# Kernel tuning notes

Measured on AMD Instinct MI355X. Metric: run time of the kernel, lower is better.

Reference implementation:

```python
import jax, jax.numpy as jnp
import numpy as np

DIM, HEADS, WS, SHIFT = 192, 6, 8, 4
EPS = 1e-5


def layer_norm(x, g, b):
    mu = jnp.mean(x, axis=-1, keepdims=True)
    var = jnp.mean(jnp.square(x - mu), axis=-1, keepdims=True)
    return (x - mu) * jax.lax.rsqrt(var + EPS) * g + b


def window_partition(x, ws):
    # x: [B, H, W, C] -> [B*nW, ws*ws, C]
    B, H, W, C = x.shape
    x = x.reshape(B, H // ws, ws, W // ws, ws, C)
    return x.transpose(0, 1, 3, 2, 4, 5).reshape(-1, ws * ws, C)


def window_merge(win, ws, B, H, W, C):
    x = win.reshape(B, H // ws, W // ws, ws, ws, C)
    return x.transpose(0, 1, 3, 2, 4, 5).reshape(B, H, W, C)


def make_shift_mask(H, W, ws, shift):
    # standard Swin attention mask for shifted windows (host-side constant)
    img = np.zeros((H, W), dtype=np.float32)
    cnt = 0
    slices = (slice(0, -ws), slice(-ws, -shift), slice(-shift, None))
    for hs in slices:
        for wsl in slices:
            img[hs, wsl] = cnt
            cnt += 1
    m = img.reshape(H // ws, ws, W // ws, ws).transpose(0, 2, 1, 3).reshape(-1, ws * ws)  # [nW, N]
    diff = m[:, None, :] - m[:, :, None]
    return jnp.asarray(np.where(diff != 0, -100.0, 0.0).astype(np.float32))  # [nW, N, N]


def swin_attention(x, qkv_w, qkv_b, proj_w, proj_b, shift):
    B, H, W, C = x.shape
    h, d = HEADS, C // HEADS
    scale = 1.0 / jnp.sqrt(jnp.asarray(d, x.dtype))
    if shift > 0:
        x = jnp.roll(x, shift=(-shift, -shift), axis=(1, 2))
    win = window_partition(x, WS)                       # [Bn, N, C]
    Bn, N, _ = win.shape
    qkv = win @ qkv_w + qkv_b                           # [Bn, N, 3C]
    qkv = qkv.reshape(Bn, N, 3, h, d).transpose(2, 0, 3, 1, 4)
    q, k, v = qkv[0], qkv[1], qkv[2]                    # [Bn, h, N, d]
    attn = jnp.einsum('bhnd,bhmd->bhnm', q, k) * scale  # [Bn, h, N, N]
    if shift > 0:
        mask = make_shift_mask(H, W, WS, shift)         # [nW, N, N]
        nW = mask.shape[0]
        attn = attn.reshape(Bn // nW, nW, h, N, N) + mask[None, :, None]
        attn = attn.reshape(Bn, h, N, N)
    attn = jax.nn.softmax(attn, axis=-1)
    out = jnp.einsum('bhnm,bhmd->bhnd', attn, v)        # [Bn, h, N, d]
    out = out.transpose(0, 2, 1, 3).reshape(Bn, N, C)
    out = out @ proj_w + proj_b
    out = window_merge(out, WS, B, H, W, C)
    if shift > 0:
        out = jnp.roll(out, shift=(shift, shift), axis=(1, 2))
    return out


def setup_inputs() -> dict:
    key = jax.random.key(0)
    ks = jax.random.split(key, 6)
    B, H, W, C = 8, 128, 128, DIM
    s = 0.02
    return {
        'x': jax.random.normal(ks[0], (B, H, W, C), jnp.float32),
        'ln1_g': jnp.ones((C,), jnp.float32),
        'ln1_b': jnp.zeros((C,), jnp.float32),
        'qkv1_w': jax.random.normal(ks[1], (C, 3 * C), jnp.float32) * s,
        'qkv1_b': jnp.zeros((3 * C,), jnp.float32),
        'proj1_w': jax.random.normal(ks[2], (C, C), jnp.float32) * s,
        'proj1_b': jnp.zeros((C,), jnp.float32),
        'ln2_g': jnp.ones((C,), jnp.float32),
        'ln2_b': jnp.zeros((C,), jnp.float32),
        'qkv2_w': jax.random.normal(ks[3], (C, 3 * C), jnp.float32) * s,
        'qkv2_b': jnp.zeros((3 * C,), jnp.float32),
        'proj2_w': jax.random.normal(ks[4], (C, C), jnp.float32) * s,
        'proj2_b': jnp.zeros((C,), jnp.float32),
    }


def reference(x, ln1_g, ln1_b, qkv1_w, qkv1_b, proj1_w, proj1_b,
              ln2_g, ln2_b, qkv2_w, qkv2_b, proj2_w, proj2_b):
    # W-MSA branch (mlp1 is an empty Sequential -> identity)
    y = layer_norm(x, ln1_g, ln1_b)
    x = x + swin_attention(y, qkv1_w, qkv1_b, proj1_w, proj1_b, shift=0)
    # SW-MSA branch (mlp2 is identity)
    y = layer_norm(x, ln2_g, ln2_b)
    x = x + swin_attention(y, qkv2_w, qkv2_b, proj2_w, proj2_b, shift=SHIFT)
    return x
```

## Files before the change

### kernel.cpp

```cpp
#include <hip/hip_runtime.h>

typedef unsigned int   u32;
typedef unsigned short u16;
typedef __bf16 bf16x8 __attribute__((ext_vector_type(8)));
typedef float  f32x4  __attribute__((ext_vector_type(4)));

__device__ __forceinline__ u16 f2bf(float f) {
    u32 u = __builtin_bit_cast(u32, f);
    u += 0x7FFFu + ((u >> 16) & 1u);
    return (u16)(u >> 16);
}
__device__ __forceinline__ u32 cvtpk(float a, float b) {
    u32 r;
    asm("v_cvt_pk_bf16_f32 %0, %1, %2" : "=v"(r) : "v"(a), "v"(b));
    return r;
}
__device__ __forceinline__ bf16x8 ldfrag(const u16* p) {
    return __builtin_bit_cast(bf16x8, *reinterpret_cast<const uint4*>(p));
}

__device__ __forceinline__ u32 swz(u32 i) { return i ^ ((i >> 3) & 7u); }

template<int SHIFT>
__global__ __launch_bounds__(768) void swin_branch(
    const float* __restrict__ xin, float* __restrict__ xout,
    const float* __restrict__ ln_g, const float* __restrict__ ln_b,
    const u16*   __restrict__ wqkv_t,
    const float* __restrict__ qkv_b,
    const u16*   __restrict__ wproj_t,
    const float* __restrict__ proj_b)
{
    __shared__ __align__(16) u16 smem[49152];
    __shared__ float red1[2][6][64];
    __shared__ float red2[2][6][64];
    constexpr u32 QOFF = 12288;
    constexpr float QSC = 0.17677669529663689f * 1.4426950408889634f;

    const int tid  = threadIdx.x;
    const int win  = (tid >= 384) ? 1 : 0;
    const int lt   = tid - win*384;
    const int wid  = lt >> 6;
    const int lane = lt & 63;
    const int lr   = lane & 15;
    const int lg   = lane >> 4;
    const u32 lsw  = swz((u32)lane);
    const u32 SB   = (u32)win * 24576u;

    const int Wid = blockIdx.x*2 + win;
    const int b   = Wid >> 8;
    const int wy  = (Wid >> 4) & 15;
    const int wx  = Wid & 15;

    {
        const int ty = lane >> 3, tx = lane & 7;
        const int shy = (wy*8 + ty + SHIFT) & 127;
        const int shx = (wx*8 + tx + SHIFT) & 127;
        const float* xp = xin + ((size_t)((b*128 + shy)*128 + shx))*192 + wid*32;
        float xv[32];
        float s1 = 0.f, s2 = 0.f;
        #pragma unroll
        for (int j = 0; j < 8; ++j) {
            float4 v = reinterpret_cast<const float4*>(xp)[j];
            xv[j*4+0]=v.x; xv[j*4+1]=v.y; xv[j*4+2]=v.z; xv[j*4+3]=v.w;
            s1 += v.x+v.y+v.z+v.w;
            s2 += v.x*v.x + v.y*v.y + v.z*v.z + v.w*v.w;
        }
        red1[win][wid][lane] = s1; red2[win][wid][lane] = s2;
        __syncthreads();
        float a1 = 0.f, a2 = 0.f;
        #pragma unroll
        for (int w = 0; w < 6; ++w) { a1 += red1[win][w][lane]; a2 += red2[win][w][lane]; }
        const float mu = a1 * (1.f/192.f);
        const float rs = rsqrtf(a2 * (1.f/192.f) - mu*mu + 1e-5f);
        const float* gp = ln_g + wid*32;
        const float* bp = ln_b + wid*32;
        const u32 yblk = SB + (u32)((lg*6 + wid)*512);
        #pragma unroll
        for (int cc8 = 0; cc8 < 4; ++cc8) {
            u32 pk[4];
            #pragma unroll
            for (int q = 0; q < 4; ++q) {
                int j = cc8*8 + q*2;
                float y0 = (xv[j]   - mu)*rs*gp[j]   + bp[j];
                float y1 = (xv[j+1] - mu)*rs*gp[j+1] + bp[j+1];
                pk[q] = cvtpk(y0, y1);
            }
            *reinterpret_cast<uint4*>(&smem[yblk + swz((u32)(lr + 16*cc8))*8]) =
                make_uint4(pk[0],pk[1],pk[2],pk[3]);
        }
    }
    __syncthreads();

    uint2 kpk[4][2];
    uint2 vpk[4][2];
    {
        {
            f32x4 acc[4][4];
            #pragma unroll
            for (int mi=0; mi<4; ++mi)
                #pragma unroll
                for (int t=0; t<4; ++t) acc[mi][t] = f32x4{0.f,0.f,0.f,0.f};
            #pragma unroll
            for (int ks=0; ks<6; ++ks) {
                bf16x8 af[4];
                #pragma unroll
                for (int mi=0; mi<4; ++mi)
                    af[mi] = ldfrag(&smem[SB + (u32)((mi*6+ks)*512) + lsw*8]);
                bf16x8 bw[4];
                #pragma unroll
                for (int t=0; t<4; ++t)
                    bw[t] = ldfrag(&wqkv_t[((t>>1)*192 + wid*32 + (t&1)*16 + lr)*192 + 32*ks + 8*lg]);
                #pragma unroll
                for (int mi=0; mi<4; ++mi)
                    #pragma unroll
                    for (int t=0; t<4; ++t)
                        acc[mi][t] = __builtin_amdgcn_mfma_f32_16x16x32_bf16(bw[t], af[mi], acc[mi][t], 0,0,0);
            }
            #pragma unroll
            for (int t=0; t<2; ++t) {
                const float4 b4 = *reinterpret_cast<const float4*>(&qkv_b[wid*32 + t*16 + 4*lg]);
                const u32 chunk = (u32)lr + 16u*(u32)(2*t + (lg>>1));
                #pragma unroll
                for (int mi=0; mi<4; ++mi) {
                    float v0 = (acc[mi][t][0] + b4.x) * QSC;
                    float v1 = (acc[mi][t][1] + b4.y) * QSC;
                    float v2 = (acc[mi][t][2] + b4.z) * QSC;
                    float v3 = (acc[mi][t][3] + b4.w) * QSC;
                    *reinterpret_cast<uint2*>(
                        &smem[SB + QOFF + (u32)(wid*2048) + mi*512 + swz(chunk)*8 + 4*(lg&1)]) =
                        make_uint2(cvtpk(v0,v1), cvtpk(v2,v3));
                }
            }
            #pragma unroll
            for (int t2=0; t2<2; ++t2) {
                const float4 b4 = *reinterpret_cast<const float4*>(&qkv_b[192 + wid*32 + t2*16 + 4*lg]);
                #pragma unroll
                for (int mi=0; mi<4; ++mi)
                    kpk[mi][t2] = make_uint2(
                        cvtpk(acc[mi][2+t2][0] + b4.x, acc[mi][2+t2][1] + b4.y),
                        cvtpk(acc[mi][2+t2][2] + b4.z, acc[mi][2+t2][3] + b4.w));
            }
        }
        {
            f32x4 acc[4][2];
            #pragma unroll
            for (int mi=0; mi<4; ++mi)
                #pragma unroll
                for (int t=0; t<2; ++t) acc[mi][t] = f32x4{0.f,0.f,0.f,0.f};
            #pragma unroll
            for (int ks=0; ks<6; ++ks) {
                bf16x8 af[4];
                #pragma unroll
                for (int mi=0; mi<4; ++mi)
                    af[mi] = ldfrag(&smem[SB + (u32)((mi*6+ks)*512) + lsw*8]);
                bf16x8 bw[2];
                #pragma unroll
                for (int t=0; t<2; ++t)
                    bw[t] = ldfrag(&wqkv_t[(384 + wid*32 + t*16 + lr)*192 + 32*ks + 8*lg]);
                #pragma unroll
                for (int mi=0; mi<4; ++mi)
                    #pragma unroll
                    for (int t=0; t<2; ++t)
                        acc[mi][t] = __builtin_amdgcn_mfma_f32_16x16x32_bf16(af[mi], bw[t], acc[mi][t], 0,0,0);
            }
            #pragma unroll
            for (int tv=0; tv<2; ++tv) {
                const float bias = qkv_b[384 + wid*32 + tv*16 + lr];
                #pragma unroll
                for (int mi=0; mi<4; ++mi)
                    vpk[mi][tv] = make_uint2(
                        cvtpk(acc[mi][tv][0] + bias, acc[mi][tv][1] + bias),
                        cvtpk(acc[mi][tv][2] + bias, acc[mi][tv][3] + bias));
            }
        }
    }
    __syncthreads();

    float rsum[4];
    f32x4 o_[2][4];
    {
        const u32 W  = SB + (u32)(wid*512);
        const u32 QB = SB + QOFF + (u32)(wid*2048);
        #define BLK(s) ((u32)(s)*3072u + W)

        #pragma unroll
        for (int t2=0; t2<2; ++t2) {
            const u32 chunk = (u32)lr + 16u*(u32)(2*t2 + (lg>>1));
            #pragma unroll
            for (int mi=0; mi<4; ++mi)
                *reinterpret_cast<uint2*>(
                    &smem[BLK(mi) + swz(chunk)*8 + 4*(lg&1)]) = kpk[mi][t2];
        }
        bf16x8 ak[4], bq[4];
        #pragma unroll
        for (int mi=0; mi<4; ++mi) ak[mi] = ldfrag(&smem[BLK(mi) + lsw*8]);
        #pragma unroll
        for (int nq=0; nq<4; ++nq) bq[nq] = ldfrag(&smem[QB + nq*512 + lsw*8]);
        __builtin_amdgcn_sched_barrier(0);

        int qcl[4];
        if constexpr (SHIFT > 0) {
            #pragma unroll
            for (int nq=0; nq<4; ++nq) {
                const int qt = 16*nq + lr;
                const int hu = wy*8 + (qt>>3);
                const int wu = wx*8 + (qt&7);
                qcl[nq] = ((hu >= 124) ? 2 : (hu >= 120 ? 1 : 0))*3
                        + ((wu >= 124) ? 2 : (wu >= 120 ? 1 : 0));
            }
        }

        uint2 p16[4][4];
        #pragma unroll
        for (int mi=0; mi<4; ++mi) {
            f32x4 sr[4];
            #pragma unroll
            for (int nq=0; nq<4; ++nq)
                sr[nq] = __builtin_amdgcn_mfma_f32_16x16x32_bf16(ak[mi], bq[nq],
                             f32x4{0.f,0.f,0.f,0.f}, 0,0,0);
            #pragma unroll
            for (int rg=0; rg<4; ++rg) {
                int kcl = 0;
                if constexpr (SHIFT > 0) {
                    const int kt = 16*mi + 4*lg + rg;
                    const int hu = wy*8 + (kt>>3);
                    const int wu = wx*8 + (kt&7);
                    kcl = ((hu >= 124) ? 2 : (hu >= 120 ? 1 : 0))*3
                        + ((wu >= 124) ? 2 : (wu >= 120 ? 1 : 0));
                }
                #pragma unroll
                for (int nq=0; nq<4; ++nq) {
                    float e = exp2f(sr[nq][rg]);
                    if constexpr (SHIFT > 0)
                        e = (kcl == qcl[nq]) ? e : 0.f;
                    sr[nq][rg] = e;
                }
            }
            #pragma unroll
            for (int nq=0; nq<4; ++nq)
                p16[mi][nq] = make_uint2(cvtpk(sr[nq][0], sr[nq][1]),
                                         cvtpk(sr[nq][2], sr[nq][3]));
        }

        #pragma unroll
        for (int mi=0; mi<4; ++mi) {
            const u32 chunk = (u32)lr + 16u*(u32)(2*(mi&1) + (lg>>1));
            #pragma unroll
            for (int nq=0; nq<4; ++nq) {
                const u32 base = (mi >> 1) ? BLK(nq) : (QB + nq*512);
                *reinterpret_cast<uint2*>(&smem[base + swz(chunk)*8 + 4*(lg&1)]) = p16[mi][nq];
            }
        }
        bf16x8 bp[4][2];
        #pragma unroll
        for (int nq=0; nq<4; ++nq) {
            bp[nq][0] = ldfrag(&smem[QB + nq*512 + lsw*8]);
            bp[nq][1] = ldfrag(&smem[BLK(nq) + lsw*8]);
        }
        __builtin_amdgcn_sched_barrier(0);

        bf16x8 aones;
        {
            const u32 one2 = 0x3F803F80u;
            aones = __builtin_bit_cast(bf16x8, make_uint4(one2, one2, one2, one2));
        }
        #pragma unroll
        for (int nq=0; nq<4; ++nq) {
            f32x4 racc = __builtin_amdgcn_mfma_f32_16x16x32_bf16(aones, bp[nq][0],
                             f32x4{0.f,0.f,0.f,0.f}, 0,0,0);
            racc = __builtin_amdgcn_mfma_f32_16x16x32_bf16(aones, bp[nq][1], racc, 0,0,0);
            rsum[nq] = __builtin_amdgcn_rcpf(racc[0]);
        }

        #pragma unroll
        for (int mi=0; mi<4; ++mi) {
            const u32 chunk = (u32)lr + 16u*(u32)(2*(mi&1) + (lg>>1));
            #pragma unroll
            for (int tv=0; tv<2; ++tv)
                *reinterpret_cast<uint2*>(
                    &smem[QB + (u32)((2*tv + (mi>>1))*512) + swz(chunk)*8 + 4*(lg&1)]) = vpk[mi][tv];
        }
        bf16x8 av[2][2];
        #pragma unroll
        for (int dv=0; dv<2; ++dv)
            #pragma unroll
            for (int ks=0; ks<2; ++ks)
                av[dv][ks] = ldfrag(&smem[QB + (u32)((2*dv + ks)*512) + lsw*8]);
        __builtin_amdgcn_sched_barrier(0);

        #pragma unroll
        for (int dv=0; dv<2; ++dv)
            #pragma unroll
            for (int nq=0; nq<4; ++nq) {
                o_[dv][nq] = __builtin_amdgcn_mfma_f32_16x16x32_bf16(av[dv][0], bp[nq][0],
                                 f32x4{0.f,0.f,0.f,0.f}, 0,0,0);
                o_[dv][nq] = __builtin_amdgcn_mfma_f32_16x16x32_bf16(av[dv][1], bp[nq][1],
                                 o_[dv][nq], 0,0,0);
            }
        __builtin_amdgcn_sched_barrier(0);

        #pragma unroll
        for (int dv=0; dv<2; ++dv) {
            const u32 chunk = (u32)lr + 16u*(u32)(2*dv + (lg>>1));
            #pragma unroll
            for (int nq=0; nq<4; ++nq) {
                const float r = rsum[nq];
                *reinterpret_cast<uint2*>(&smem[BLK(nq) + swz(chunk)*8 + 4*(lg&1)]) =
                    make_uint2(cvtpk(o_[dv][nq][0]*r, o_[dv][nq][1]*r),
                               cvtpk(o_[dv][nq][2]*r, o_[dv][nq][3]*r));
            }
        }
        #undef BLK
    }
    __syncthreads();

    {
        f32x4 a2[4][2];
        #pragma unroll
        for (int mi=0; mi<4; ++mi)
            #pragma unroll
            for (int ni=0; ni<2; ++ni) a2[mi][ni] = f32x4{0.f,0.f,0.f,0.f};
        #pragma unroll
        for (int ks=0; ks<6; ++ks) {
            bf16x8 af[4], bw[2];
            #pragma unroll
            for (int mi=0; mi<4; ++mi)
                af[mi] = ldfrag(&smem[SB + (u32)((mi*6+ks)*512) + lsw*8]);
            #pragma unroll
            for (int ni=0; ni<2; ++ni)
                bw[ni] = ldfrag(&wproj_t[(wid*32 + 16*ni + lr)*192 + 32*ks + 8*lg]);
            #pragma unroll
            for (int mi=0; mi<4; ++mi)
                #pragma unroll
                for (int ni=0; ni<2; ++ni)
                    a2[mi][ni] = __builtin_amdgcn_mfma_f32_16x16x32_bf16(af[mi], bw[ni], a2[mi][ni], 0,0,0);
        }
        #pragma unroll
        for (int ni=0; ni<2; ++ni) {
            const int c  = wid*32 + 16*ni + lr;
            const float pb = proj_b[c];
            #pragma unroll
            for (int mi=0; mi<4; ++mi)
                #pragma unroll
                for (int rg=0; rg<4; ++rg) {
                    const int row = 16*mi + 4*lg + rg;
                    const int ty = row >> 3, tx = row & 7;
                    const int shy = (wy*8 + ty + SHIFT) & 127;
                    const int shx = (wx*8 + tx + SHIFT) & 127;
                    const size_t idx = ((size_t)((b*128 + shy)*128 + shx))*192 + c;
                    xout[idx] = xin[idx] + a2[mi][ni][rg] + pb;
                }
        }
    }
}

__global__ void prep_weights(const float* __restrict__ qkv1, const float* __restrict__ proj1,
                             const float* __restrict__ qkv2, const float* __restrict__ proj2,
                             u16* __restrict__ ws)
{
    const int i = blockIdx.x*blockDim.x + threadIdx.x;
    if (i < 110592) {
        const int n = i / 192, k = i - n*192;
        ws[i]          = f2bf(qkv1[k*576 + n]);
        ws[147456 + i] = f2bf(qkv2[k*576 + n]);
    }
    if (i < 36864) {
        const int n = i / 192, k = i - n*192;
        ws[110592 + i] = f2bf(proj1[k*192 + n]);
        ws[258048 + i] = f2bf(proj2[k*192 + n]);
    }
}

extern "C" void kernel_launch(void* const* d_in, const int* in_sizes, int n_in,
                              void* d_out, int out_size, void* d_ws, size_t ws_size,
                              hipStream_t stream)
{
    const float* x       = (const float*)d_in[0];
    const float* ln1_g   = (const float*)d_in[1];
    const float* ln1_b   = (const float*)d_in[2];
    const float* qkv1_w  = (const float*)d_in[3];
    const float* qkv1_b  = (const float*)d_in[4];
    const float* proj1_w = (const float*)d_in[5];
    const float* proj1_b = (const float*)d_in[6];
    const float* ln2_g   = (const float*)d_in[7];
    const float* ln2_b   = (const float*)d_in[8];
    const float* qkv2_w  = (const float*)d_in[9];
    const float* qkv2_b  = (const float*)d_in[10];
    const float* proj2_w = (const float*)d_in[11];
    const float* proj2_b = (const float*)d_in[12];
    float* out = (float*)d_out;
    u16*   wsp = (u16*)d_ws;

    prep_weights<<<dim3(432), dim3(256), 0, stream>>>(qkv1_w, proj1_w, qkv2_w, proj2_w, wsp);
    swin_branch<0><<<dim3(1024), dim3(768), 0, stream>>>(x,   out, ln1_g, ln1_b,
                                                         wsp,        qkv1_b, wsp+110592, proj1_b);
    swin_branch<4><<<dim3(1024), dim3(768), 0, stream>>>(out, out, ln2_g, ln2_b,
                                                         wsp+147456, qkv2_b, wsp+258048, proj2_b);
}
```

Baseline: 262.8 us.

## Make Swin branch kernel persistent and prefetch next window's input

Shrinks the grid from 1024 to 256 blocks. Each block now loops over 4 window pairs in turn. During the output-projection phase of one iteration, it issues the global loads of x for the next window pair into registers, so LayerNorm input latency overlaps with MFMA work. This removes block launch and prologue repetition, but keeps more live registers across the loop and serialises work per CU.

```diff
diff --git a/kernel.cpp b/kernel.cpp
--- a/kernel.cpp
+++ b/kernel.cpp
@@ -46,310 +46,331 @@
     const u32 lsw  = swz((u32)lane);
     const u32 SB   = (u32)win * 24576u;
 
-    const int Wid = blockIdx.x*2 + win;
-    const int b   = Wid >> 8;
-    const int wy  = (Wid >> 4) & 15;
-    const int wx  = Wid & 15;
-
+    const int ty = lane >> 3, tx = lane & 7;
+
+    float4 xv4[8];
     {
-        const int ty = lane >> 3, tx = lane & 7;
-        const int shy = (wy*8 + ty + SHIFT) & 127;
-        const int shx = (wx*8 + tx + SHIFT) & 127;
-        const float* xp = xin + ((size_t)((b*128 + shy)*128 + shx))*192 + wid*32;
-        float xv[32];
-        float s1 = 0.f, s2 = 0.f;
+        const int Wid = (int)blockIdx.x*2 + win;
+        const int b0=Wid>>8, wy0=(Wid>>4)&15, wx0=Wid&15;
+        const int shy=(wy0*8+ty+SHIFT)&127, shx=(wx0*8+tx+SHIFT)&127;
+        const float* xp = xin + ((size_t)((b0*128+shy)*128+shx))*192 + wid*32;
         #pragma unroll
-        for (int j = 0; j < 8; ++j) {
-            float4 v = reinterpret_cast<const float4*>(xp)[j];
-            xv[j*4+0]=v.x; xv[j*4+1]=v.y; xv[j*4+2]=v.z; xv[j*4+3]=v.w;
-            s1 += v.x+v.y+v.z+v.w;
-            s2 += v.x*v.x + v.y*v.y + v.z*v.z + v.w*v.w;
-        }
-        red1[win][wid][lane] = s1; red2[win][wid][lane] = s2;
+        for (int j=0;j<8;++j) xv4[j] = reinterpret_cast<const float4*>(xp)[j];
+    }
+
+    #pragma unroll 1
+    for (int it = 0; it < 4; ++it) {
+        const int Wid = (it*256 + (int)blockIdx.x)*2 + win;
+        const int b   = Wid >> 8;
+        const int wy  = (Wid >> 4) & 15;
+        const int wx  = Wid & 15;
+
+        {
+            float s1 = 0.f, s2 = 0.f;
+            #pragma unroll
+            for (int j = 0; j < 8; ++j) {
+                float4 v = xv4[j];
+                s1 += v.x+v.y+v.z+v.w;
+                s2 += v.x*v.x + v.y*v.y + v.z*v.z + v.w*v.w;
+            }
+            red1[win][wid][lane] = s1; red2[win][wid][lane] = s2;
+        }
         __syncthreads();
-        float a1 = 0.f, a2 = 0.f;
-        #pragma unroll
-        for (int w = 0; w < 6; ++w) { a1 += red1[win][w][lane]; a2 += red2[win][w][lane]; }
-        const float mu = a1 * (1.f/192.f);
-        const float rs = rsqrtf(a2 * (1.f/192.f) - mu*mu + 1e-5f);
-        const float* gp = ln_g + wid*32;
-        const float* bp = ln_b + wid*32;
-        const u32 yblk = SB + (u32)((lg*6 + wid)*512);
-        #pragma unroll
-        for (int cc8 = 0; cc8 < 4; ++cc8) {
-            u32 pk[4];
-            #pragma unroll
-            for (int q = 0; q < 4; ++q) {
-                int j = cc8*8 + q*2;
-                float y0 = (xv[j]   - mu)*rs*gp[j]   + bp[j];
-                float y1 = (xv[j+1] - mu)*rs*gp[j+1] + bp[j+1];
-                pk[q] = cvtpk(y0, y1);
-            }
-            *reinterpret_cast<uint4*>(&smem[yblk + swz((u32)(lr + 16*cc8))*8]) =
-                make_uint4(pk[0],pk[1],pk[2],pk[3]);
-        }
-    }
-    __syncthreads();
-
-    uint2 kpk[4][2];
-    uint2 vpk[4][2];
-    {
         {
-            f32x4 acc[4][4];
+            float a1 = 0.f, a2 = 0.f;
+            #pragma unroll
+            for (int w = 0; w < 6; ++w) { a1 += red1[win][w][lane]; a2 += red2[win][w][lane]; }
+            const float mu = a1 * (1.f/192.f);
+            const float rs = rsqrtf(a2 * (1.f/192.f) - mu*mu + 1e-5f);
+            const float* gp = ln_g + wid*32;
+            const float* bp = ln_b + wid*32;
+            const float* xf = reinterpret_cast<const float*>(xv4);
+            const u32 yblk = SB + (u32)((lg*6 + wid)*512);
+            #pragma unroll
+            for (int cc8 = 0; cc8 < 4; ++cc8) {
+                u32 pk[4];
+                #pragma unroll
+                for (int q = 0; q < 4; ++q) {
+                    int j = cc8*8 + q*2;
+                    float y0 = (xf[j]   - mu)*rs*gp[j]   + bp[j];
+                    float y1 = (xf[j+1] - mu)*rs*gp[j+1] + bp[j+1];
+                    pk[q] = cvtpk(y0, y1);
+                }
+                *reinterpret_cast<uint4*>(&smem[yblk + swz((u32)(lr + 16*cc8))*8]) =
+                    make_uint4(pk[0],pk[1],pk[2],pk[3]);
+            }
+        }
+        __syncthreads();
+
+        uint2 kpk[4][2];
+        uint2 vpk[4][2];
+        {
+            {
+                f32x4 acc[4][4];
+                #pragma unroll
+                for (int mi=0; mi<4; ++mi)
+                    #pragma unroll
+                    for (int t=0; t<4; ++t) acc[mi][t] = f32x4{0.f,0.f,0.f,0.f};
+                #pragma unroll
+                for (int ks=0; ks<6; ++ks) {
+                    bf16x8 af[4];
+                    #pragma unroll
+                    for (int mi=0; mi<4; ++mi)
+                        af[mi] = ldfrag(&smem[SB + (u32)((mi*6+ks)*512) + lsw*8]);
+                    bf16x8 bw[4];
+                    #pragma unroll
+                    for (int t=0; t<4; ++t)
+                        bw[t] = ldfrag(&wqkv_t[((t>>1)*192 + wid*32 + (t&1)*16 + lr)*192 + 32*ks + 8*lg]);
+                    #pragma unroll
+                    for (int mi=0; mi<4; ++mi)
+                        #pragma unroll
+                        for (int t=0; t<4; ++t)
+                            acc[mi][t] = __builtin_amdgcn_mfma_f32_16x16x32_bf16(bw[t], af[mi], acc[mi][t], 0,0,0);
+                }
+                #pragma unroll
+                for (int t=0; t<2; ++t) {
+                    const float4 b4 = *reinterpret_cast<const float4*>(&qkv_b[wid*32 + t*16 + 4*lg]);
+                    const u32 chunk = (u32)lr + 16u*(u32)(2*t + (lg>>1));
+                    #pragma unroll
+                    for (int mi=0; mi<4; ++mi) {
+                        float v0 = (acc[mi][t][0] + b4.x) * QSC;
+                        float v1 = (acc[mi][t][1] + b4.y) * QSC;
+                        float v2 = (acc[mi][t][2] + b4.z) * QSC;
+                        float v3 = (acc[mi][t][3] + b4.w) * QSC;
+                        *reinterpret_cast<uint2*>(
+                            &smem[SB + QOFF + (u32)(wid*2048) + mi*512 + swz(chunk)*8 + 4*(lg&1)]) =
+                            make_uint2(cvtpk(v0,v1), cvtpk(v2,v3));
+                    }
+                }
+                #pragma unroll
+                for (int t2=0; t2<2; ++t2) {
+                    const float4 b4 = *reinterpret_cast<const float4*>(&qkv_b[192 + wid*32 + t2*16 + 4*lg]);
+                    #pragma unroll
+                    for (int mi=0; mi<4; ++mi)
+                        kpk[mi][t2] = make_uint2(
+                            cvtpk(acc[mi][2+t2][0] + b4.x, acc[mi][2+t2][1] + b4.y),
+                            cvtpk(acc[mi][2+t2][2] + b4.z, acc[mi][2+t2][3] + b4.w));
+                }
+            }
+            {
+                f32x4 acc[4][2];
+                #pragma unroll
+                for (int mi=0; mi<4; ++mi)
+                    #pragma unroll
+                    for (int t=0; t<2; ++t) acc[mi][t] = f32x4{0.f,0.f,0.f,0.f};
+                #pragma unroll
+                for (int ks=0; ks<6; ++ks) {
+                    bf16x8 af[4];
+                    #pragma unroll
+                    for (int mi=0; mi<4; ++mi)
+                        af[mi] = ldfrag(&smem[SB + (u32)((mi*6+ks)*512) + lsw*8]);
+                    bf16x8 bw[2];
+                    #pragma unroll
+                    for (int t=0; t<2; ++t)
+                        bw[t] = ldfrag(&wqkv_t[(384 + wid*32 + t*16 + lr)*192 + 32*ks + 8*lg]);
+                    #pragma unroll
+                    for (int mi=0; mi<4; ++mi)
+                        #pragma unroll
+                        for (int t=0; t<2; ++t)
+                            acc[mi][t] = __builtin_amdgcn_mfma_f32_16x16x32_bf16(af[mi], bw[t], acc[mi][t], 0,0,0);
+                }
+                #pragma unroll
+                for (int tv=0; tv<2; ++tv) {
+                    const float bias = qkv_b[384 + wid*32 + tv*16 + lr];
+                    #pragma unroll
+                    for (int mi=0; mi<4; ++mi)
+                        vpk[mi][tv] = make_uint2(
+                            cvtpk(acc[mi][tv][0] + bias, acc[mi][tv][1] + bias),
+                            cvtpk(acc[mi][tv][2] + bias, acc[mi][tv][3] + bias));
+                }
+            }
+        }
+        __syncthreads();
+
+        float rsum[4];
+        f32x4 o_[2][4];
+        {
+            const u32 W  = SB + (u32)(wid*512);
+            const u32 QB = SB + QOFF + (u32)(wid*2048);
+            #define BLK(s) ((u32)(s)*3072u + W)
+
+            #pragma unroll
+            for (int t2=0; t2<2; ++t2) {
+                const u32 chunk = (u32)lr + 16u*(u32)(2*t2 + (lg>>1));
+                #pragma unroll
+                for (int mi=0; mi<4; ++mi)
+                    *reinterpret_cast<uint2*>(
+                        &smem[BLK(mi) + swz(chunk)*8 + 4*(lg&1)]) = kpk[mi][t2];
+            }
+            bf16x8 ak[4], bq[4];
+            #pragma unroll
+            for (int mi=0; mi<4; ++mi) ak[mi] = ldfrag(&smem[BLK(mi) + lsw*8]);
+            #pragma unroll
+            for (int nq=0; nq<4; ++nq) bq[nq] = ldfrag(&smem[QB + nq*512 + lsw*8]);
+            __builtin_amdgcn_sched_barrier(0);
+
+            int qcl[4];
+            if constexpr (SHIFT > 0) {
+                #pragma unroll
+                for (int nq=0; nq<4; ++nq) {
+                    const int qt = 16*nq + lr;
+                    const int hu = wy*8 + (qt>>3);
+                    const int wu = wx*8 + (qt&7);
+                    qcl[nq] = ((hu >= 124) ? 2 : (hu >= 120 ? 1 : 0))*3
+                            + ((wu >= 124) ? 2 : (wu >= 120 ? 1 : 0));
+                }
+            }
+
+            uint2 p16[4][4];
+            #pragma unroll
+            for (int mi=0; mi<4; ++mi) {
+                f32x4 sr[4];
+                #pragma unroll
+                for (int nq=0; nq<4; ++nq)
+                    sr[nq] = __builtin_amdgcn_mfma_f32_16x16x32_bf16(ak[mi], bq[nq],
+                                 f32x4{0.f,0.f,0.f,0.f}, 0,0,0);
+                #pragma unroll
+                for (int rg=0; rg<4; ++rg) {
+                    int kcl = 0;
+                    if constexpr (SHIFT > 0) {
+                        const int kt = 16*mi + 4*lg + rg;
+                        const int hu = wy*8 + (kt>>3);
+                        const int wu = wx*8 + (kt&7);
+                        kcl = ((hu >= 124) ? 2 : (hu >= 120 ? 1 : 0))*3
+                            + ((wu >= 124) ? 2 : (wu >= 120 ? 1 : 0));
+                    }
+                    #pragma unroll
+                    for (int nq=0; nq<4; ++nq) {
+                        float e = exp2f(sr[nq][rg]);
+                        if constexpr (SHIFT > 0)
+                            e = (kcl == qcl[nq]) ? e : 0.f;
+                        sr[nq][rg] = e;
+                    }
+                }
+                #pragma unroll
+                for (int nq=0; nq<4; ++nq)
+                    p16[mi][nq] = make_uint2(cvtpk(sr[nq][0], sr[nq][1]),
+                                             cvtpk(sr[nq][2], sr[nq][3]));
+            }
+
+            #pragma unroll
+            for (int mi=0; mi<4; ++mi) {
+                const u32 chunk = (u32)lr + 16u*(u32)(2*(mi&1) + (lg>>1));
+                #pragma unroll
+                for (int nq=0; nq<4; ++nq) {
+                    const u32 base = (mi >> 1) ? BLK(nq) : (QB + nq*512);
+                    *reinterpret_cast<uint2*>(&smem[base + swz(chunk)*8 + 4*(lg&1)]) = p16[mi][nq];
+                }
+            }
+            bf16x8 bp[4][2];
+            #pragma unroll
+            for (int nq=0; nq<4; ++nq) {
+                bp[nq][0] = ldfrag(&smem[QB + nq*512 + lsw*8]);
+                bp[nq][1] = ldfrag(&smem[BLK(nq) + lsw*8]);
+            }
+            __builtin_amdgcn_sched_barrier(0);
+
+            bf16x8 aones;
+            {
+                const u32 one2 = 0x3F803F80u;
+                aones = __builtin_bit_cast(bf16x8, make_uint4(one2, one2, one2, one2));
+            }
+            #pragma unroll
+            for (int nq=0; nq<4; ++nq) {
+                f32x4 racc = __builtin_amdgcn_mfma_f32_16x16x32_bf16(aones, bp[nq][0],
+                                 f32x4{0.f,0.f,0.f,0.f}, 0,0,0);
+                racc = __builtin_amdgcn_mfma_f32_16x16x32_bf16(aones, bp[nq][1], racc, 0,0,0);
+                rsum[nq] = __builtin_amdgcn_rcpf(racc[0]);
+            }
+
+            #pragma unroll
+            for (int mi=0; mi<4; ++mi) {
+                const u32 chunk = (u32)lr + 16u*(u32)(2*(mi&1) + (lg>>1));
+                #pragma unroll
+                for (int tv=0; tv<2; ++tv)
+                    *reinterpret_cast<uint2*>(
+                        &smem[QB + (u32)((2*tv + (mi>>1))*512) + swz(chunk)*8 + 4*(lg&1)]) = vpk[mi][tv];
+            }
+            bf16x8 av[2][2];
+            #pragma unroll
+            for (int dv=0; dv<2; ++dv)
+                #pragma unroll
+                for (int ks=0; ks<2; ++ks)
+                    av[dv][ks] = ldfrag(&smem[QB + (u32)((2*dv + ks)*512) + lsw*8]);
+            __builtin_amdgcn_sched_barrier(0);
+
+            #pragma unroll
+            for (int dv=0; dv<2; ++dv)
+                #pragma unroll
+                for (int nq=0; nq<4; ++nq) {
+                    o_[dv][nq] = __builtin_amdgcn_mfma_f32_16x16x32_bf16(av[dv][0], bp[nq][0],
+                                     f32x4{0.f,0.f,0.f,0.f}, 0,0,0);
+                    o_[dv][nq] = __builtin_amdgcn_mfma_f32_16x16x32_bf16(av[dv][1], bp[nq][1],
+                                     o_[dv][nq], 0,0,0);
+                }
+            __builtin_amdgcn_sched_barrier(0);
+
+            #pragma unroll
+            for (int dv=0; dv<2; ++dv) {
+                const u32 chunk = (u32)lr + 16u*(u32)(2*dv + (lg>>1));
+                #pragma unroll
+                for (int nq=0; nq<4; ++nq) {
+                    const float r = rsum[nq];
+                    *reinterpret_cast<uint2*>(&smem[BLK(nq) + swz(chunk)*8 + 4*(lg&1)]) =
+                        make_uint2(cvtpk(o_[dv][nq][0]*r, o_[dv][nq][1]*r),
+                                   cvtpk(o_[dv][nq][2]*r, o_[dv][nq][3]*r));
+                }
+            }
+            #undef BLK
+        }
+        __syncthreads();
+
+        if (it < 3) {
+            const int WidN = ((it+1)*256 + (int)blockIdx.x)*2 + win;
+            const int bn=WidN>>8, wyn=(WidN>>4)&15, wxn=WidN&15;
+            const int shy=(wyn*8+ty+SHIFT)&127, shx=(wxn*8+tx+SHIFT)&127;
+            const float* xp = xin + ((size_t)((bn*128+shy)*128+shx))*192 + wid*32;
+            #pragma unroll
+            for (int j=0;j<8;++j) xv4[j] = reinterpret_cast<const float4*>(xp)[j];
+        }
+
+        {
+            f32x4 a2[4][2];
             #pragma unroll
             for (int mi=0; mi<4; ++mi)
                 #pragma unroll
-                for (int t=0; t<4; ++t) acc[mi][t] = f32x4{0.f,0.f,0.f,0.f};
+                for (int ni=0; ni<2; ++ni) a2[mi][ni] = f32x4{0.f,0.f,0.f,0.f};
             #pragma unroll
             for (int ks=0; ks<6; ++ks) {
-                bf16x8 af[4];
+                bf16x8 af[4], bw[2];
                 #pragma unroll
                 for (int mi=0; mi<4; ++mi)
                     af[mi] = ldfrag(&smem[SB + (u32)((mi*6+ks)*512) + lsw*8]);
-                bf16x8 bw[4];
-                #pragma unroll
-                for (int t=0; t<4; ++t)
-                    bw[t] = ldfrag(&wqkv_t[((t>>1)*192 + wid*32 + (t&1)*16 + lr)*192 + 32*ks + 8*lg]);
-                #pragma unroll
-                for (int mi=0; mi<4; ++mi)
-                    #pragma unroll
-                    for (int t=0; t<4; ++t)
-                        acc[mi][t] = __builtin_amdgcn_mfma_f32_16x16x32_bf16(bw[t], af[mi], acc[mi][t], 0,0,0);
-            }
-            #pragma unroll
-            for (int t=0; t<2; ++t) {
-                const float4 b4 = *reinterpret_cast<const float4*>(&qkv_b[wid*32 + t*16 + 4*lg]);
-                const u32 chunk = (u32)lr + 16u*(u32)(2*t + (lg>>1));
-                #pragma unroll
-                for (int mi=0; mi<4; ++mi) {
-                    float v0 = (acc[mi][t][0] + b4.x) * QSC;
-                    float v1 = (acc[mi][t][1] + b4.y) * QSC;
-                    float v2 = (acc[mi][t][2] + b4.z) * QSC;
-                    float v3 = (acc[mi][t][3] + b4.w) * QSC;
-                    *reinterpret_cast<uint2*>(
-                        &smem[SB + QOFF + (u32)(wid*2048) + mi*512 + swz(chunk)*8 + 4*(lg&1)]) =
-                        make_uint2(cvtpk(v0,v1), cvtpk(v2,v3));
-                }
-            }
-            #pragma unroll
-            for (int t2=0; t2<2; ++t2) {
-                const float4 b4 = *reinterpret_cast<const float4*>(&qkv_b[192 + wid*32 + t2*16 + 4*lg]);
-                #pragma unroll
-                for (int mi=0; mi<4; ++mi)
-                    kpk[mi][t2] = make_uint2(
-                        cvtpk(acc[mi][2+t2][0] + b4.x, acc[mi][2+t2][1] + b4.y),
-                        cvtpk(acc[mi][2+t2][2] + b4.z, acc[mi][2+t2][3] + b4.w));
-            }
-        }
-        {
-            f32x4 acc[4][2];
-            #pragma unroll
-            for (int mi=0; mi<4; ++mi)
-                #pragma unroll
-                for (int t=0; t<2; ++t) acc[mi][t] = f32x4{0.f,0.f,0.f,0.f};
-            #pragma unroll
-            for (int ks=0; ks<6; ++ks) {
-                bf16x8 af[4];
-                #pragma unroll
-                for (int mi=0; mi<4; ++mi)
-                    af[mi] = ldfrag(&smem[SB + (u32)((mi*6+ks)*512) + lsw*8]);
-                bf16x8 bw[2];
-                #pragma unroll
-                for (int t=0; t<2; ++t)
-                    bw[t] = ldfrag(&wqkv_t[(384 + wid*32 + t*16 + lr)*192 + 32*ks + 8*lg]);
-                #pragma unroll
-                for (int mi=0; mi<4; ++mi)
-                    #pragma unroll
-                    for (int t=0; t<2; ++t)
-                        acc[mi][t] = __builtin_amdgcn_mfma_f32_16x16x32_bf16(af[mi], bw[t], acc[mi][t], 0,0,0);
-            }
-            #pragma unroll
-            for (int tv=0; tv<2; ++tv) {
-                const float bias = qkv_b[384 + wid*32 + tv*16 + lr];
-                #pragma unroll
-                for (int mi=0; mi<4; ++mi)
-                    vpk[mi][tv] = make_uint2(
-                        cvtpk(acc[mi][tv][0] + bias, acc[mi][tv][1] + bias),
-                        cvtpk(acc[mi][tv][2] + bias, acc[mi][tv][3] + bias));
-            }
-        }
-    }
-    __syncthreads();
-
-    float rsum[4];
-    f32x4 o_[2][4];
-    {
-        const u32 W  = SB + (u32)(wid*512);
-        const u32 QB = SB + QOFF + (u32)(wid*2048);
-        #define BLK(s) ((u32)(s)*3072u + W)
-
-        #pragma unroll
-        for (int t2=0; t2<2; ++t2) {
-            const u32 chunk = (u32)lr + 16u*(u32)(2*t2 + (lg>>1));
-            #pragma unroll
-            for (int mi=0; mi<4; ++mi)
-                *reinterpret_cast<uint2*>(
-                    &smem[BLK(mi) + swz(chunk)*8 + 4*(lg&1)]) = kpk[mi][t2];
-        }
-        bf16x8 ak[4], bq[4];
-        #pragma unroll
-        for (int mi=0; mi<4; ++mi) ak[mi] = ldfrag(&smem[BLK(mi) + lsw*8]);
-        #pragma unroll
-        for (int nq=0; nq<4; ++nq) bq[nq] = ldfrag(&smem[QB + nq*512 + lsw*8]);
-        __builtin_amdgcn_sched_barrier(0);
-
-        int qcl[4];
-        if constexpr (SHIFT > 0) {
-            #pragma unroll
-            for (int nq=0; nq<4; ++nq) {
-                const int qt = 16*nq + lr;
-                const int hu = wy*8 + (qt>>3);
-                const int wu = wx*8 + (qt&7);
-                qcl[nq] = ((hu >= 124) ? 2 : (hu >= 120 ? 1 : 0))*3
-                        + ((wu >= 124) ? 2 : (wu >= 120 ? 1 : 0));
-            }
-        }
-
-        uint2 p16[4][4];
-        #pragma unroll
-        for (int mi=0; mi<4; ++mi) {
-            f32x4 sr[4];
-            #pragma unroll
-            for (int nq=0; nq<4; ++nq)
-                sr[nq] = __builtin_amdgcn_mfma_f32_16x16x32_bf16(ak[mi], bq[nq],
-                             f32x4{0.f,0.f,0.f,0.f}, 0,0,0);
-            #pragma unroll
-            for (int rg=0; rg<4; ++rg) {
-                int kcl = 0;
-                if constexpr (SHIFT > 0) {
-                    const int kt = 16*mi + 4*lg + rg;
-                    const int hu = wy*8 + (kt>>3);
-                    const int wu = wx*8 + (kt&7);
-                    kcl = ((hu >= 124) ? 2 : (hu >= 120 ? 1 : 0))*3
-                        + ((wu >= 124) ? 2 : (wu >= 120 ? 1 : 0));
-                }
-                #pragma unroll
-                for (int nq=0; nq<4; ++nq) {
-                    float e = exp2f(sr[nq][rg]);
-                    if constexpr (SHIFT > 0)
-                        e = (kcl == qcl[nq]) ? e : 0.f;
-                    sr[nq][rg] = e;
-                }
-            }
-            #pragma unroll
-            for (int nq=0; nq<4; ++nq)
-                p16[mi][nq] = make_uint2(cvtpk(sr[nq][0], sr[nq][1]),
-                                         cvtpk(sr[nq][2], sr[nq][3]));
-        }
-
-        #pragma unroll
-        for (int mi=0; mi<4; ++mi) {
-            const u32 chunk = (u32)lr + 16u*(u32)(2*(mi&1) + (lg>>1));
-            #pragma unroll
-            for (int nq=0; nq<4; ++nq) {
-                const u32 base = (mi >> 1) ? BLK(nq) : (QB + nq*512);
-                *reinterpret_cast<uint2*>(&smem[base + swz(chunk)*8 + 4*(lg&1)]) = p16[mi][nq];
-            }
-        }
-        bf16x8 bp[4][2];
-        #pragma unroll
-        for (int nq=0; nq<4; ++nq) {
-            bp[nq][0] = ldfrag(&smem[QB + nq*512 + lsw*8]);
-            bp[nq][1] = ldfrag(&smem[BLK(nq) + lsw*8]);
-        }
-        __builtin_amdgcn_sched_barrier(0);
-
-        bf16x8 aones;
-        {
-            const u32 one2 = 0x3F803F80u;
-            aones = __builtin_bit_cast(bf16x8, make_uint4(one2, one2, one2, one2));
-        }
-        #pragma unroll
-        for (int nq=0; nq<4; ++nq) {
-            f32x4 racc = __builtin_amdgcn_mfma_f32_16x16x32_bf16(aones, bp[nq][0],
-                             f32x4{0.f,0.f,0.f,0.f}, 0,0,0);
-            racc = __builtin_amdgcn_mfma_f32_16x16x32_bf16(aones, bp[nq][1], racc, 0,0,0);
-            rsum[nq] = __builtin_amdgcn_rcpf(racc[0]);
-        }
-
-        #pragma unroll
-        for (int mi=0; mi<4; ++mi) {
-            const u32 chunk = (u32)lr + 16u*(u32)(2*(mi&1) + (lg>>1));
-            #pragma unroll
-            for (int tv=0; tv<2; ++tv)
-                *reinterpret_cast<uint2*>(
-                    &smem[QB + (u32)((2*tv + (mi>>1))*512) + swz(chunk)*8 + 4*(lg&1)]) = vpk[mi][tv];
-        }
-        bf16x8 av[2][2];
-        #pragma unroll
-        for (int dv=0; dv<2; ++dv)
-            #pragma unroll
-            for (int ks=0; ks<2; ++ks)
-                av[dv][ks] = ldfrag(&smem[QB + (u32)((2*dv + ks)*512) + lsw*8]);
-        __builtin_amdgcn_sched_barrier(0);
-
-        #pragma unroll
-        for (int dv=0; dv<2; ++dv)
-            #pragma unroll
-            for (int nq=0; nq<4; ++nq) {
-                o_[dv][nq] = __builtin_amdgcn_mfma_f32_16x16x32_bf16(av[dv][0], bp[nq][0],
-                                 f32x4{0.f,0.f,0.f,0.f}, 0,0,0);
-                o_[dv][nq] = __builtin_amdgcn_mfma_f32_16x16x32_bf16(av[dv][1], bp[nq][1],
-                                 o_[dv][nq], 0,0,0);
-            }
-        __builtin_amdgcn_sched_barrier(0);
-
-        #pragma unroll
-        for (int dv=0; dv<2; ++dv) {
-            const u32 chunk = (u32)lr + 16u*(u32)(2*dv + (lg>>1));
-            #pragma unroll
-            for (int nq=0; nq<4; ++nq) {
-                const float r = rsum[nq];
-                *reinterpret_cast<uint2*>(&smem[BLK(nq) + swz(chunk)*8 + 4*(lg&1)]) =
-                    make_uint2(cvtpk(o_[dv][nq][0]*r, o_[dv][nq][1]*r),
-                               cvtpk(o_[dv][nq][2]*r, o_[dv][nq][3]*r));
-            }
-        }
-        #undef BLK
-    }
-    __syncthreads();
-
-    {
-        f32x4 a2[4][2];
-        #pragma unroll
-        for (int mi=0; mi<4; ++mi)
-            #pragma unroll
-            for (int ni=0; ni<2; ++ni) a2[mi][ni] = f32x4{0.f,0.f,0.f,0.f};
-        #pragma unroll
-        for (int ks=0; ks<6; ++ks) {
-            bf16x8 af[4], bw[2];
-            #pragma unroll
-            for (int mi=0; mi<4; ++mi)
-                af[mi] = ldfrag(&smem[SB + (u32)((mi*6+ks)*512) + lsw*8]);
-            #pragma unroll
-            for (int ni=0; ni<2; ++ni)
-                bw[ni] = ldfrag(&wproj_t[(wid*32 + 16*ni + lr)*192 + 32*ks + 8*lg]);
-            #pragma unroll
-            for (int mi=0; mi<4; ++mi)
                 #pragma unroll
                 for (int ni=0; ni<2; ++ni)
-                    a2[mi][ni] = __builtin_amdgcn_mfma_f32_16x16x32_bf16(af[mi], bw[ni], a2[mi][ni], 0,0,0);
-        }
-        #pragma unroll
-        for (int ni=0; ni<2; ++ni) {
-            const int c  = wid*32 + 16*ni + lr;
-            const float pb = proj_b[c];
-            #pragma unroll
-            for (int mi=0; mi<4; ++mi)
-                #pragma unroll
-                for (int rg=0; rg<4; ++rg) {
-                    const int row = 16*mi + 4*lg + rg;
-                    const int ty = row >> 3, tx = row & 7;
-                    const int shy = (wy*8 + ty + SHIFT) & 127;
-                    const int shx = (wx*8 + tx + SHIFT) & 127;
-                    const size_t idx = ((size_t)((b*128 + shy)*128 + shx))*192 + c;
-                    xout[idx] = xin[idx] + a2[mi][ni][rg] + pb;
-                }
+                    bw[ni] = ldfrag(&wproj_t[(wid*32 + 16*ni + lr)*192 + 32*ks + 8*lg]);
+                #pragma unroll
+                for (int mi=0; mi<4; ++mi)
+                    #pragma unroll
+                    for (int ni=0; ni<2; ++ni)
+                        a2[mi][ni] = __builtin_amdgcn_mfma_f32_16x16x32_bf16(af[mi], bw[ni], a2[mi][ni], 0,0,0);
+            }
+            #pragma unroll
+            for (int ni=0; ni<2; ++ni) {
+                const int c  = wid*32 + 16*ni + lr;
+                const float pb = proj_b[c];
+                #pragma unroll
+                for (int mi=0; mi<4; ++mi)
+                    #pragma unroll
+                    for (int rg=0; rg<4; ++rg) {
+                        const int row = 16*mi + 4*lg + rg;
+                        const int ty2 = row >> 3, tx2 = row & 7;
+                        const int shy = (wy*8 + ty2 + SHIFT) & 127;
+                        const int shx = (wx*8 + tx2 + SHIFT) & 127;
+                        const size_t idx = ((size_t)((b*128 + shy)*128 + shx))*192 + c;
+                        xout[idx] = xin[idx] + a2[mi][ni][rg] + pb;
+                    }
+            }
         }
     }
 }
@@ -392,8 +413,8 @@
     u16*   wsp = (u16*)d_ws;
 
     prep_weights<<<dim3(432), dim3(256), 0, stream>>>(qkv1_w, proj1_w, qkv2_w, proj2_w, wsp);
-    swin_branch<0><<<dim3(1024), dim3(768), 0, stream>>>(x,   out, ln1_g, ln1_b,
-                                                         wsp,        qkv1_b, wsp+110592, proj1_b);
-    swin_branch<4><<<dim3(1024), dim3(768), 0, stream>>>(out, out, ln2_g, ln2_b,
-                                                         wsp+147456, qkv2_b, wsp+258048, proj2_b);
-}
+    swin_branch<0><<<dim3(256), dim3(768), 0, stream>>>(x,   out, ln1_g, ln1_b,
+                                                        wsp,        qkv1_b, wsp+110592, proj1_b);
+    swin_branch<4><<<dim3(256), dim3(768), 0, stream>>>(out, out, ln2_g, ln2_b,
+                                                        wsp+147456, qkv2_b, wsp+258048, proj2_b);
+}
```

Result: slower. 369.5 us (+40.6%).

## Use one window per 384-thread block and split Q/K GEMM to cut registers

Applied to the files above, without the earlier changes.

Each block now handles a single attention window with 6 waves instead of two windows with 12 waves. Shared memory per block is halved and the grid doubles. The fused Q+K projection, which held 16 accumulator tiles, is split into separate Q and K passes of 8 tiles each, and launch bounds now request 4 blocks per CU. The aim is lower register pressure and higher occupancy, at the cost of reloading the LN activation fragments from LDS once more.

```diff
diff --git a/kernel.cpp b/kernel.cpp
--- a/kernel.cpp
+++ b/kernel.cpp
@@ -22,7 +22,7 @@
 __device__ __forceinline__ u32 swz(u32 i) { return i ^ ((i >> 3) & 7u); }
 
 template<int SHIFT>
-__global__ __launch_bounds__(768) void swin_branch(
+__global__ __launch_bounds__(384, 4) void swin_branch(
     const float* __restrict__ xin, float* __restrict__ xout,
     const float* __restrict__ ln_g, const float* __restrict__ ln_b,
     const u16*   __restrict__ wqkv_t,
@@ -30,23 +30,20 @@
     const u16*   __restrict__ wproj_t,
     const float* __restrict__ proj_b)
 {
-    __shared__ __align__(16) u16 smem[49152];
-    __shared__ float red1[2][6][64];
-    __shared__ float red2[2][6][64];
+    __shared__ __align__(16) u16 smem[24576];
+    __shared__ float red1[6][64];
+    __shared__ float red2[6][64];
     constexpr u32 QOFF = 12288;
     constexpr float QSC = 0.17677669529663689f * 1.4426950408889634f;
 
     const int tid  = threadIdx.x;
-    const int win  = (tid >= 384) ? 1 : 0;
-    const int lt   = tid - win*384;
-    const int wid  = lt >> 6;
-    const int lane = lt & 63;
+    const int wid  = tid >> 6;
+    const int lane = tid & 63;
     const int lr   = lane & 15;
     const int lg   = lane >> 4;
     const u32 lsw  = swz((u32)lane);
-    const u32 SB   = (u32)win * 24576u;
-
-    const int Wid = blockIdx.x*2 + win;
+
+    const int Wid = blockIdx.x;
     const int b   = Wid >> 8;
     const int wy  = (Wid >> 4) & 15;
     const int wx  = Wid & 15;
@@ -65,16 +62,16 @@
             s1 += v.x+v.y+v.z+v.w;
             s2 += v.x*v.x + v.y*v.y + v.z*v.z + v.w*v.w;
         }
-        red1[win][wid][lane] = s1; red2[win][wid][lane] = s2;
+        red1[wid][lane] = s1; red2[wid][lane] = s2;
         __syncthreads();
         float a1 = 0.f, a2 = 0.f;
         #pragma unroll
-        for (int w = 0; w < 6; ++w) { a1 += red1[win][w][lane]; a2 += red2[win][w][lane]; }
+        for (int w = 0; w < 6; ++w) { a1 += red1[w][lane]; a2 += red2[w][lane]; }
         const float mu = a1 * (1.f/192.f);
         const float rs = rsqrtf(a2 * (1.f/192.f) - mu*mu + 1e-5f);
         const float* gp = ln_g + wid*32;
         const float* bp = ln_b + wid*32;
-        const u32 yblk = SB + (u32)((lg*6 + wid)*512);
+        const u32 yblk = (u32)((lg*6 + wid)*512);
         #pragma unroll
         for (int cc8 = 0; cc8 < 4; ++cc8) {
             u32 pk[4];
@@ -95,25 +92,25 @@
     uint2 vpk[4][2];
     {
         {
-            f32x4 acc[4][4];
-            #pragma unroll
-            for (int mi=0; mi<4; ++mi)
-                #pragma unroll
-                for (int t=0; t<4; ++t) acc[mi][t] = f32x4{0.f,0.f,0.f,0.f};
+            f32x4 acc[4][2];
+            #pragma unroll
+            for (int mi=0; mi<4; ++mi)
+                #pragma unroll
+                for (int t=0; t<2; ++t) acc[mi][t] = f32x4{0.f,0.f,0.f,0.f};
             #pragma unroll
             for (int ks=0; ks<6; ++ks) {
                 bf16x8 af[4];
                 #pragma unroll
                 for (int mi=0; mi<4; ++mi)
-                    af[mi] = ldfrag(&smem[SB + (u32)((mi*6+ks)*512) + lsw*8]);
-                bf16x8 bw[4];
-                #pragma unroll
-                for (int t=0; t<4; ++t)
-                    bw[t] = ldfrag(&wqkv_t[((t>>1)*192 + wid*32 + (t&1)*16 + lr)*192 + 32*ks + 8*lg]);
+                    af[mi] = ldfrag(&smem[(u32)((mi*6+ks)*512) + lsw*8]);
+                bf16x8 bw[2];
+                #pragma unroll
+                for (int t=0; t<2; ++t)
+                    bw[t] = ldfrag(&wqkv_t[(wid*32 + t*16 + lr)*192 + 32*ks + 8*lg]);
                 #pragma unroll
                 for (int mi=0; mi<4; ++mi)
                     #pragma unroll
-                    for (int t=0; t<4; ++t)
+                    for (int t=0; t<2; ++t)
                         acc[mi][t] = __builtin_amdgcn_mfma_f32_16x16x32_bf16(bw[t], af[mi], acc[mi][t], 0,0,0);
             }
             #pragma unroll
@@ -127,18 +124,41 @@
                     float v2 = (acc[mi][t][2] + b4.z) * QSC;
                     float v3 = (acc[mi][t][3] + b4.w) * QSC;
                     *reinterpret_cast<uint2*>(
-                        &smem[SB + QOFF + (u32)(wid*2048) + mi*512 + swz(chunk)*8 + 4*(lg&1)]) =
+                        &smem[QOFF + (u32)(wid*2048) + mi*512 + swz(chunk)*8 + 4*(lg&1)]) =
                         make_uint2(cvtpk(v0,v1), cvtpk(v2,v3));
                 }
             }
+        }
+        {
+            f32x4 acc[4][2];
+            #pragma unroll
+            for (int mi=0; mi<4; ++mi)
+                #pragma unroll
+                for (int t=0; t<2; ++t) acc[mi][t] = f32x4{0.f,0.f,0.f,0.f};
+            #pragma unroll
+            for (int ks=0; ks<6; ++ks) {
+                bf16x8 af[4];
+                #pragma unroll
+                for (int mi=0; mi<4; ++mi)
+                    af[mi] = ldfrag(&smem[(u32)((mi*6+ks)*512) + lsw*8]);
+                bf16x8 bw[2];
+                #pragma unroll
+                for (int t=0; t<2; ++t)
+                    bw[t] = ldfrag(&wqkv_t[(192 + wid*32 + t*16 + lr)*192 + 32*ks + 8*lg]);
+                #pragma unroll
+                for (int mi=0; mi<4; ++mi)
+                    #pragma unroll
+                    for (int t=0; t<2; ++t)
+                        acc[mi][t] = __builtin_amdgcn_mfma_f32_16x16x32_bf16(bw[t], af[mi], acc[mi][t], 0,0,0);
+            }
             #pragma unroll
             for (int t2=0; t2<2; ++t2) {
                 const float4 b4 = *reinterpret_cast<const float4*>(&qkv_b[192 + wid*32 + t2*16 + 4*lg]);
                 #pragma unroll
                 for (int mi=0; mi<4; ++mi)
                     kpk[mi][t2] = make_uint2(
-                        cvtpk(acc[mi][2+t2][0] + b4.x, acc[mi][2+t2][1] + b4.y),
-                        cvtpk(acc[mi][2+t2][2] + b4.z, acc[mi][2+t2][3] + b4.w));
+                        cvtpk(acc[mi][t2][0] + b4.x, acc[mi][t2][1] + b4.y),
+                        cvtpk(acc[mi][t2][2] + b4.z, acc[mi][t2][3] + b4.w));
             }
         }
         {
@@ -152,7 +172,7 @@
                 bf16x8 af[4];
                 #pragma unroll
                 for (int mi=0; mi<4; ++mi)
-                    af[mi] = ldfrag(&smem[SB + (u32)((mi*6+ks)*512) + lsw*8]);
+                    af[mi] = ldfrag(&smem[(u32)((mi*6+ks)*512) + lsw*8]);
                 bf16x8 bw[2];
                 #pragma unroll
                 for (int t=0; t<2; ++t)
@@ -179,8 +199,8 @@
     float rsum[4];
     f32x4 o_[2][4];
     {
-        const u32 W  = SB + (u32)(wid*512);
-        const u32 QB = SB + QOFF + (u32)(wid*2048);
+        const u32 W  = (u32)(wid*512);
+        const u32 QB = QOFF + (u32)(wid*2048);
         #define BLK(s) ((u32)(s)*3072u + W)
 
         #pragma unroll
@@ -325,7 +345,7 @@
             bf16x8 af[4], bw[2];
             #pragma unroll
             for (int mi=0; mi<4; ++mi)
-                af[mi] = ldfrag(&smem[SB + (u32)((mi*6+ks)*512) + lsw*8]);
+                af[mi] = ldfrag(&smem[(u32)((mi*6+ks)*512) + lsw*8]);
             #pragma unroll
             for (int ni=0; ni<2; ++ni)
                 bw[ni] = ldfrag(&wproj_t[(wid*32 + 16*ni + lr)*192 + 32*ks + 8*lg]);
@@ -392,8 +412,8 @@
     u16*   wsp = (u16*)d_ws;
 
     prep_weights<<<dim3(432), dim3(256), 0, stream>>>(qkv1_w, proj1_w, qkv2_w, proj2_w, wsp);
-    swin_branch<0><<<dim3(1024), dim3(768), 0, stream>>>(x,   out, ln1_g, ln1_b,
+    swin_branch<0><<<dim3(2048), dim3(384), 0, stream>>>(x,   out, ln1_g, ln1_b,
                                                          wsp,        qkv1_b, wsp+110592, proj1_b);
-    swin_branch<4><<<dim3(1024), dim3(768), 0, stream>>>(out, out, ln2_g, ln2_b,
+    swin_branch<4><<<dim3(2048), dim3(384), 0, stream>>>(out, out, ln2_g, ln2_b,
                                                          wsp+147456, qkv2_b, wsp+258048, proj2_b);
 }
```

Result: slower. 379.6 us (+44.4%).
